# Optimization experiments

Measured on AMD Instinct MI355X. Metric: run time of the kernel, lower is better.

## Reference

```python
import jax, jax.numpy as jnp
import numpy as np

N_NODES = 100000


def gcn_conv(x, edge_index, W, b):
    """PyG GCNConv: linear transform, add self-loops, sym-normalized scatter-add, bias."""
    n = x.shape[0]
    h = x @ W  # [N, out]
    loop = jnp.arange(n, dtype=edge_index.dtype)
    src = jnp.concatenate([edge_index[0], loop])
    dst = jnp.concatenate([edge_index[1], loop])
    deg = jax.ops.segment_sum(jnp.ones_like(dst, dtype=h.dtype), dst, num_segments=n)
    dinv = jnp.where(deg > 0, jax.lax.rsqrt(jnp.maximum(deg, 1.0)), 0.0)
    norm = dinv[src] * dinv[dst]  # [E+N]
    msg = norm[:, None] * h[src]  # gather + scale
    out = jax.ops.segment_sum(msg, dst, num_segments=n)  # scatter-add
    return out + b


def setup_inputs() -> dict:
    key = jax.random.key(0)
    k1, k2, k3, k4 = jax.random.split(key, 4)
    in_f, gnn_f, out_f = 128, 64, 40
    n_edges = 1600000
    x = jax.random.normal(k1, (N_NODES, in_f), dtype=jnp.float32)
    edge_index = jax.random.randint(k2, (2, n_edges), 0, N_NODES, dtype=jnp.int64)
    W1 = jax.random.normal(k3, (in_f, gnn_f), dtype=jnp.float32) * (in_f ** -0.5)
    b1 = jnp.zeros((gnn_f,), dtype=jnp.float32)
    W2 = jax.random.normal(k4, (gnn_f, out_f), dtype=jnp.float32) * (gnn_f ** -0.5)
    b2 = jnp.zeros((out_f,), dtype=jnp.float32)
    return {"x": x, "edge_index": edge_index, "W1": W1, "b1": b1, "W2": W2, "b2": b2}


def reference(x, edge_index, W1, b1, W2, b2):
    h = gcn_conv(x, edge_index, W1, b1)
    h = jax.nn.relu(h)  # Dropout is identity in eval mode
    out = gcn_conv(h, edge_index, W2, b2)
    return out
```

## Files before the change

### kernel.cpp

```cpp
#include <hip/hip_runtime.h>


__device__ inline float bflo(unsigned u) { return __uint_as_float(u << 16); }
__device__ inline float bfhi(unsigned u) { return __uint_as_float(u & 0xffff0000u); }
__device__ inline unsigned short f2bf(float x) {
    unsigned u = __float_as_uint(x);
    return (unsigned short)((u + 0x7fff + ((u >> 16) & 1)) >> 16);
}

#define NBINS 256
#define EPB   2048

__global__ __launch_bounds__(256) void p1_hist(const int* __restrict__ dst, int e,
                                               int nblk, int* __restrict__ hist_t) {
    __shared__ int h[NBINS];
    int tid = threadIdx.x;
    h[tid] = 0;
    __syncthreads();
    int base = blockIdx.x * EPB;
    #pragma unroll
    for (int j = 0; j < 8; ++j) {
        int idx = base + j * 256 + tid;
        if (idx < e) atomicAdd(&h[dst[idx] >> 9], 1);
    }
    __syncthreads();
    hist_t[tid * nblk + blockIdx.x] = h[tid];
}

__global__ __launch_bounds__(256) void scan_a(const int* __restrict__ in, int* __restrict__ part,
                                              int* __restrict__ aux, int n) {
    __shared__ int lds[256];
    int tid = threadIdx.x;
    int base = blockIdx.x * 1024 + tid * 4;
    int v0 = (base + 0 < n) ? in[base + 0] : 0;
    int v1 = (base + 1 < n) ? in[base + 1] : 0;
    int v2 = (base + 2 < n) ? in[base + 2] : 0;
    int v3 = (base + 3 < n) ? in[base + 3] : 0;
    int s = v0 + v1 + v2 + v3;
    lds[tid] = s;
    __syncthreads();
    for (int off = 1; off < 256; off <<= 1) {
        int t = (tid >= off) ? lds[tid - off] : 0;
        __syncthreads();
        lds[tid] += t;
        __syncthreads();
    }
    int excl = lds[tid] - s;
    if (base + 0 < n) part[base + 0] = excl;
    if (base + 1 < n) part[base + 1] = excl + v0;
    if (base + 2 < n) part[base + 2] = excl + v0 + v1;
    if (base + 3 < n) part[base + 3] = excl + v0 + v1 + v2;
    if (tid == 255) aux[blockIdx.x] = lds[255];
}

__global__ __launch_bounds__(256) void scan_b(int* __restrict__ aux, int nb) {
    __shared__ int lds[256];
    int tid = threadIdx.x;
    int v = (tid < nb) ? aux[tid] : 0;
    lds[tid] = v;
    __syncthreads();
    for (int off = 1; off < 256; off <<= 1) {
        int t = (tid >= off) ? lds[tid - off] : 0;
        __syncthreads();
        lds[tid] += t;
        __syncthreads();
    }
    if (tid < nb) aux[tid] = lds[tid] - v;
}

__global__ __launch_bounds__(256) void scan_c(int* __restrict__ data,
                                              const int* __restrict__ aux, int n) {
    int i = blockIdx.x * blockDim.x + threadIdx.x;
    if (i < n) data[i] += aux[i >> 10];
}

__global__ __launch_bounds__(256) void p1_scatter(const int* __restrict__ src,
                                                  const int* __restrict__ dst, int e,
                                                  int nblk, const int* __restrict__ off_t,
                                                  unsigned* __restrict__ ebuf) {
    __shared__ int cur[NBINS];
    int tid = threadIdx.x;
    cur[tid] = off_t[tid * nblk + blockIdx.x];
    __syncthreads();
    int base = blockIdx.x * EPB;
    #pragma unroll
    for (int j = 0; j < 8; ++j) {
        int idx = base + j * 256 + tid;
        if (idx < e) {
            int d = dst[idx];
            int p = atomicAdd(&cur[d >> 9], 1);
            ebuf[p] = (unsigned)src[idx] | ((unsigned)(d & 511) << 17);
        }
    }
}

__global__ __launch_bounds__(256) void p2_build(const unsigned* __restrict__ ebuf,
                                                const int* __restrict__ off_t,
                                                int nblk, int e, int n, int nbg,
                                                int* __restrict__ row_off,
                                                int* __restrict__ ssrc,
                                                float* __restrict__ dinv) {
    __shared__ int cnt[512];
    __shared__ int s1[256];
    __shared__ int loc[512];
    int tid = threadIdx.x;
    int g = blockIdx.x;
    int node0 = g << 9;
    int nlocal = n - node0; if (nlocal > 512) nlocal = 512;

    int segstart = off_t[g * nblk];
    int segend   = (g + 1 < NBINS) ? off_t[(g + 1) * nblk] : e;

    cnt[tid] = 0; cnt[tid + 256] = 0;
    __syncthreads();

    for (int i = segstart + tid; i < segend; i += 256)
        atomicAdd(&cnt[ebuf[i] >> 17], 1);
    __syncthreads();

    int a0 = cnt[2 * tid], a1 = cnt[2 * tid + 1];
    int sp = a0 + a1;
    s1[tid] = sp;
    __syncthreads();
    for (int off = 1; off < 256; off <<= 1) {
        int t = (tid >= off) ? s1[tid - off] : 0;
        __syncthreads();
        s1[tid] += t;
        __syncthreads();
    }
    int excl = s1[tid] - sp;
    loc[2 * tid]     = excl;
    loc[2 * tid + 1] = excl + a0;
    __syncthreads();

    for (int l = tid; l < nlocal; l += 256) {
        row_off[node0 + l] = segstart + loc[l];
        dinv[node0 + l] = rsqrtf((float)cnt[l] + 1.0f);
    }
    if (g == nbg - 1 && tid == 0) row_off[n] = segend;
    __syncthreads();

    for (int i = segstart + tid; i < segend; i += 256) {
        unsigned p = ebuf[i];
        int r = atomicAdd(&loc[p >> 17], 1);
        ssrc[segstart + r] = (int)(p & 0x1FFFFu);
    }
}

template <int K, int M>
__global__ __launch_bounds__(256) void gemm_xw(const float* __restrict__ X,
                                               const float* __restrict__ W,
                                               const float* __restrict__ dinv,
                                               unsigned short* __restrict__ G, int n) {
    constexpr int GQ = 8;
    constexpr int SG = GQ + 1;
    __shared__ float4 xs[64 * SG];
    __shared__ float4 wt[64 * SG];

    const int tid = threadIdx.x;
    const int r0  = blockIdx.x * 64;
    const int tc  = tid & 15;
    const int tr  = tid >> 4;

    const int srow0 = tid >> 3, skq0 = tid & 7;
    const int srow1 = (tid + 256) >> 3, skq1 = tid & 7;
    int rr0 = r0 + srow0; rr0 = rr0 < n ? rr0 : n - 1;
    int rr1 = r0 + srow1; rr1 = rr1 < n ? rr1 : n - 1;

    float acc[4][4];
    #pragma unroll
    for (int i = 0; i < 4; ++i)
        #pragma unroll
        for (int j = 0; j < 4; ++j) acc[i][j] = 0.f;

    for (int kc = 0; kc < K; kc += 32) {
        __syncthreads();
        xs[srow0 * SG + skq0] = *reinterpret_cast<const float4*>(&X[(size_t)rr0 * K + kc + skq0 * 4]);
        xs[srow1 * SG + skq1] = *reinterpret_cast<const float4*>(&X[(size_t)rr1 * K + kc + skq1 * 4]);
        {
            int m = srow0, kq = skq0;
            float4 v = make_float4(0.f, 0.f, 0.f, 0.f);
            if (m < M) {
                int k = kc + kq * 4;
                v.x = W[(k + 0) * M + m]; v.y = W[(k + 1) * M + m];
                v.z = W[(k + 2) * M + m]; v.w = W[(k + 3) * M + m];
            }
            wt[m * SG + kq] = v;
            m = srow1; kq = skq1;
            float4 u = make_float4(0.f, 0.f, 0.f, 0.f);
            if (m < M) {
                int k = kc + kq * 4;
                u.x = W[(k + 0) * M + m]; u.y = W[(k + 1) * M + m];
                u.z = W[(k + 2) * M + m]; u.w = W[(k + 3) * M + m];
            }
            wt[m * SG + kq] = u;
        }
        __syncthreads();

        #pragma unroll 2
        for (int kq = 0; kq < GQ; ++kq) {
            float4 xv[4], wv[4];
            #pragma unroll
            for (int i = 0; i < 4; ++i) xv[i] = xs[(tr + 16 * i) * SG + kq];
            #pragma unroll
            for (int j = 0; j < 4; ++j) wv[j] = wt[(tc + 16 * j) * SG + kq];
            #pragma unroll
            for (int i = 0; i < 4; ++i)
                #pragma unroll
                for (int j = 0; j < 4; ++j) {
                    acc[i][j] = fmaf(xv[i].x, wv[j].x, acc[i][j]);
                    acc[i][j] = fmaf(xv[i].y, wv[j].y, acc[i][j]);
                    acc[i][j] = fmaf(xv[i].z, wv[j].z, acc[i][j]);
                    acc[i][j] = fmaf(xv[i].w, wv[j].w, acc[i][j]);
                }
        }
    }

    #pragma unroll
    for (int i = 0; i < 4; ++i) {
        int row = r0 + tr + 16 * i;
        if (row < n) {
            float di = dinv[row];
            #pragma unroll
            for (int j = 0; j < 4; ++j) {
                int col = tc + 16 * j;
                if (col < M) G[(size_t)row * M + col] = f2bf(di * acc[i][j]);
            }
        }
    }
}

template <bool RELU>
__global__ __launch_bounds__(256) void aggregate64(const unsigned short* __restrict__ G,
                                                   const float* __restrict__ dinv,
                                                   const int* __restrict__ row_off,
                                                   const int* __restrict__ ssrc,
                                                   const float* __restrict__ bias,
                                                   float* __restrict__ out, int n) {
    int wid  = (blockIdx.x * blockDim.x + threadIdx.x) >> 6;
    if (wid >= n) return;
    int lane = threadIdx.x & 63;
    int g = lane >> 3;
    int c = lane & 7;
    const uint4* __restrict__ G16 = (const uint4*)G;

    float acc[8];
    #pragma unroll
    for (int k = 0; k < 8; ++k) acc[k] = 0.f;

    int e0 = row_off[wid], e1 = row_off[wid + 1];
    int e = e0 + g;
    for (; e + 8 < e1; e += 16) {
        int s0 = ssrc[e], s1 = ssrc[e + 8];
        uint4 u0 = G16[(size_t)s0 * 8 + c];
        uint4 u1 = G16[(size_t)s1 * 8 + c];
        acc[0] += bflo(u0.x); acc[1] += bfhi(u0.x);
        acc[2] += bflo(u0.y); acc[3] += bfhi(u0.y);
        acc[4] += bflo(u0.z); acc[5] += bfhi(u0.z);
        acc[6] += bflo(u0.w); acc[7] += bfhi(u0.w);
        acc[0] += bflo(u1.x); acc[1] += bfhi(u1.x);
        acc[2] += bflo(u1.y); acc[3] += bfhi(u1.y);
        acc[4] += bflo(u1.z); acc[5] += bfhi(u1.z);
        acc[6] += bflo(u1.w); acc[7] += bfhi(u1.w);
    }
    if (e < e1) {
        int s = ssrc[e];
        uint4 u = G16[(size_t)s * 8 + c];
        acc[0] += bflo(u.x); acc[1] += bfhi(u.x);
        acc[2] += bflo(u.y); acc[3] += bfhi(u.y);
        acc[4] += bflo(u.z); acc[5] += bfhi(u.z);
        acc[6] += bflo(u.w); acc[7] += bfhi(u.w);
    }

    #pragma unroll
    for (int k = 0; k < 8; ++k) acc[k] += __shfl_xor(acc[k], 8);
    #pragma unroll
    for (int k = 0; k < 8; ++k) acc[k] += __shfl_xor(acc[k], 16);
    #pragma unroll
    for (int k = 0; k < 8; ++k) acc[k] += __shfl_xor(acc[k], 32);

    float di = dinv[wid];
    uint4 gs = G16[(size_t)wid * 8 + c];
    float4 b0 = ((const float4*)bias)[2 * c];
    float4 b1 = ((const float4*)bias)[2 * c + 1];
    float4 o0, o1;
    o0.x = fmaf(di, acc[0] + bflo(gs.x), b0.x);
    o0.y = fmaf(di, acc[1] + bfhi(gs.x), b0.y);
    o0.z = fmaf(di, acc[2] + bflo(gs.y), b0.z);
    o0.w = fmaf(di, acc[3] + bfhi(gs.y), b0.w);
    o1.x = fmaf(di, acc[4] + bflo(gs.z), b1.x);
    o1.y = fmaf(di, acc[5] + bfhi(gs.z), b1.y);
    o1.z = fmaf(di, acc[6] + bflo(gs.w), b1.z);
    o1.w = fmaf(di, acc[7] + bfhi(gs.w), b1.w);
    if (RELU) {
        o0.x = fmaxf(o0.x, 0.f); o0.y = fmaxf(o0.y, 0.f);
        o0.z = fmaxf(o0.z, 0.f); o0.w = fmaxf(o0.w, 0.f);
        o1.x = fmaxf(o1.x, 0.f); o1.y = fmaxf(o1.y, 0.f);
        o1.z = fmaxf(o1.z, 0.f); o1.w = fmaxf(o1.w, 0.f);
    }
    if (g == 0) {
        ((float4*)out)[(size_t)wid * 16 + 2 * c]     = o0;
        ((float4*)out)[(size_t)wid * 16 + 2 * c + 1] = o1;
    }
}

template <bool RELU>
__global__ __launch_bounds__(256) void aggregate40(const unsigned short* __restrict__ G,
                                                   const float* __restrict__ dinv,
                                                   const int* __restrict__ row_off,
                                                   const int* __restrict__ ssrc,
                                                   const float* __restrict__ bias,
                                                   float* __restrict__ out, int n) {
    constexpr int MH = 20;
    int wid  = (blockIdx.x * blockDim.x + threadIdx.x) >> 6;
    if (wid >= n) return;
    int lane = threadIdx.x & 63;
    int half = lane >> 5;
    int c    = lane & 31;
    int cc   = c < MH ? c : MH - 1;
    const unsigned* __restrict__ G2 = (const unsigned*)G;

    float2 acc = make_float2(0.f, 0.f);
    int e0 = row_off[wid], e1 = row_off[wid + 1];

    int e = e0 + half;
    for (; e + 6 < e1; e += 8) {
        int s0 = ssrc[e], s1 = ssrc[e + 2], s2 = ssrc[e + 4], s3 = ssrc[e + 6];
        unsigned g0 = G2[(size_t)s0 * MH + cc];
        unsigned g1 = G2[(size_t)s1 * MH + cc];
        unsigned g2 = G2[(size_t)s2 * MH + cc];
        unsigned g3 = G2[(size_t)s3 * MH + cc];
        acc.x += bflo(g0); acc.y += bfhi(g0);
        acc.x += bflo(g1); acc.y += bfhi(g1);
        acc.x += bflo(g2); acc.y += bfhi(g2);
        acc.x += bflo(g3); acc.y += bfhi(g3);
    }
    for (; e < e1; e += 2) {
        unsigned g = G2[(size_t)ssrc[e] * MH + cc];
        acc.x += bflo(g); acc.y += bfhi(g);
    }

    acc.x += __shfl_xor(acc.x, 32);
    acc.y += __shfl_xor(acc.y, 32);

    float di = dinv[wid];
    unsigned gs = G2[(size_t)wid * MH + cc];
    float2 bv = ((const float2*)bias)[cc];
    float o0 = fmaf(di, acc.x + bflo(gs), bv.x);
    float o1 = fmaf(di, acc.y + bfhi(gs), bv.y);
    if (RELU) { o0 = fmaxf(o0, 0.f); o1 = fmaxf(o1, 0.f); }
    if (half == 0 && c < MH) {
        ((float2*)out)[(size_t)wid * MH + c] = make_float2(o0, o1);
    }
}

extern "C" void kernel_launch(void* const* d_in, const int* in_sizes, int n_in,
                              void* d_out, int out_size, void* d_ws, size_t ws_size,
                              hipStream_t stream) {
    const float* x  = (const float*)d_in[0];
    const int*   ei = (const int*)d_in[1];
    const float* W1 = (const float*)d_in[2];
    const float* b1 = (const float*)d_in[3];
    const float* W2 = (const float*)d_in[4];
    const float* b2 = (const float*)d_in[5];

    const int gnn_f = in_sizes[3];
    const int out_f = in_sizes[5];
    const int in_f  = in_sizes[2] / gnn_f;
    const int e     = in_sizes[1] / 2;
    const int n     = in_sizes[0] / in_f;

    const int* src = ei;
    const int* dst = ei + e;

    const int nblk   = (e + EPB - 1) / EPB;
    const int nscan  = NBINS * nblk;
    const int nbg    = (n + 511) / 512;
    const int nchunks = (nscan + 1023) / 1024;

    char* base = (char*)d_ws;
    size_t off = 0;
    auto alloc = [&](size_t bytes) -> char* {
        char* p = base + off;
        off = (off + bytes + 255) & ~(size_t)255;
        return p;
    };
    int*            hist_t  = (int*)            alloc((size_t)nscan * 4);
    int*            off_t   = (int*)            alloc((size_t)nscan * 4);
    int*            aux     = (int*)            alloc(256 * 4);
    unsigned*       ebuf    = (unsigned*)       alloc((size_t)e * 4);
    int*            row_off = (int*)            alloc((size_t)(n + 1) * 4);
    int*            ssrc    = (int*)            alloc((size_t)e * 4);
    float*          dinv    = (float*)          alloc((size_t)n * 4);
    unsigned short* g1      = (unsigned short*) alloc((size_t)n * gnn_f * 2);
    float*          a1      = (float*)          alloc((size_t)n * gnn_f * 4);
    unsigned short* g2      = (unsigned short*) alloc((size_t)n * out_f * 2);
    (void)ws_size;

    p1_hist<<<nblk, 256, 0, stream>>>(dst, e, nblk, hist_t);
    scan_a<<<nchunks, 256, 0, stream>>>(hist_t, off_t, aux, nscan);
    scan_b<<<1, 256, 0, stream>>>(aux, nchunks);
    scan_c<<<(nscan + 255) / 256, 256, 0, stream>>>(off_t, aux, nscan);
    p1_scatter<<<nblk, 256, 0, stream>>>(src, dst, e, nblk, off_t, ebuf);
    p2_build<<<nbg, 256, 0, stream>>>(ebuf, off_t, nblk, e, n, nbg, row_off, ssrc, dinv);

    gemm_xw<128, 64><<<(n + 63) / 64, 256, 0, stream>>>(x, W1, dinv, g1, n);
    aggregate64<true><<<(n + 3) / 4, 256, 0, stream>>>(g1, dinv, row_off, ssrc, b1, a1, n);

    gemm_xw<64, 40><<<(n + 63) / 64, 256, 0, stream>>>(a1, W2, dinv, g2, n);
    aggregate40<false><<<(n + 3) / 4, 256, 0, stream>>>(g2, dinv, row_off, ssrc, b2, (float*)d_out, n);
}
```

Before: 289.8 us.

## Split feature columns into slices so aggregation gathers hit cache-resident tables

The GEMM now writes its bf16 output in column-sliced layout: 4 slices of 16 features for layer 1 and 2 slices of 20 for layer 2. Each aggregation launches one grid per slice, so every pass gathers from a smaller table that is more likely to stay in L2 or the last-level cache. The cost is that edge indices and row offsets are re-read once per slice, each gather is narrower (4-byte instead of 16-byte loads), and more blocks are launched.

Result: slower. 399.7 us (+38.0%).

```diff
diff --git a/kernel.cpp b/kernel.cpp
--- a/kernel.cpp
+++ b/kernel.cpp
@@ -147,7 +147,7 @@
     }
 }
 
-template <int K, int M>
+template <int K, int M, int SF>
 __global__ __launch_bounds__(256) void gemm_xw(const float* __restrict__ X,
                                                const float* __restrict__ W,
                                                const float* __restrict__ dinv,
@@ -223,135 +223,111 @@
             float di = dinv[row];
             #pragma unroll
             for (int j = 0; j < 4; ++j) {
-                int col = tc + 16 * j;
-                if (col < M) G[(size_t)row * M + col] = f2bf(di * acc[i][j]);
+                int cc = tc + 16 * j;
+                if (cc < M) {
+                    int s  = cc / SF;
+                    int lc = cc - s * SF;
+                    G[(size_t)s * n * SF + (size_t)row * SF + lc] = f2bf(di * acc[i][j]);
+                }
             }
         }
     }
 }
 
 template <bool RELU>
-__global__ __launch_bounds__(256) void aggregate64(const unsigned short* __restrict__ G,
-                                                   const float* __restrict__ dinv,
-                                                   const int* __restrict__ row_off,
-                                                   const int* __restrict__ ssrc,
-                                                   const float* __restrict__ bias,
-                                                   float* __restrict__ out, int n) {
-    int wid  = (blockIdx.x * blockDim.x + threadIdx.x) >> 6;
+__global__ __launch_bounds__(256) void aggregate64s(const unsigned* __restrict__ G,
+                                                    const float* __restrict__ dinv,
+                                                    const int* __restrict__ row_off,
+                                                    const int* __restrict__ ssrc,
+                                                    const float* __restrict__ bias,
+                                                    float* __restrict__ out, int n) {
+    int bps   = (n + 3) >> 2;
+    int slice = blockIdx.x / bps;
+    int blk   = blockIdx.x - slice * bps;
+    int wid   = (blk * 256 + (int)threadIdx.x) >> 6;
     if (wid >= n) return;
     int lane = threadIdx.x & 63;
     int g = lane >> 3;
     int c = lane & 7;
-    const uint4* __restrict__ G16 = (const uint4*)G;
-
-    float acc[8];
-    #pragma unroll
-    for (int k = 0; k < 8; ++k) acc[k] = 0.f;
-
+    const unsigned* __restrict__ Gs = G + (size_t)slice * n * 8;
+
+    float2 acc = make_float2(0.f, 0.f);
     int e0 = row_off[wid], e1 = row_off[wid + 1];
     int e = e0 + g;
     for (; e + 8 < e1; e += 16) {
         int s0 = ssrc[e], s1 = ssrc[e + 8];
-        uint4 u0 = G16[(size_t)s0 * 8 + c];
-        uint4 u1 = G16[(size_t)s1 * 8 + c];
-        acc[0] += bflo(u0.x); acc[1] += bfhi(u0.x);
-        acc[2] += bflo(u0.y); acc[3] += bfhi(u0.y);
-        acc[4] += bflo(u0.z); acc[5] += bfhi(u0.z);
-        acc[6] += bflo(u0.w); acc[7] += bfhi(u0.w);
-        acc[0] += bflo(u1.x); acc[1] += bfhi(u1.x);
-        acc[2] += bflo(u1.y); acc[3] += bfhi(u1.y);
-        acc[4] += bflo(u1.z); acc[5] += bfhi(u1.z);
-        acc[6] += bflo(u1.w); acc[7] += bfhi(u1.w);
+        unsigned u0 = Gs[(size_t)s0 * 8 + c];
+        unsigned u1 = Gs[(size_t)s1 * 8 + c];
+        acc.x += bflo(u0); acc.y += bfhi(u0);
+        acc.x += bflo(u1); acc.y += bfhi(u1);
     }
     if (e < e1) {
-        int s = ssrc[e];
-        uint4 u = G16[(size_t)s * 8 + c];
-        acc[0] += bflo(u.x); acc[1] += bfhi(u.x);
-        acc[2] += bflo(u.y); acc[3] += bfhi(u.y);
-        acc[4] += bflo(u.z); acc[5] += bfhi(u.z);
-        acc[6] += bflo(u.w); acc[7] += bfhi(u.w);
-    }
-
-    #pragma unroll
-    for (int k = 0; k < 8; ++k) acc[k] += __shfl_xor(acc[k], 8);
-    #pragma unroll
-    for (int k = 0; k < 8; ++k) acc[k] += __shfl_xor(acc[k], 16);
-    #pragma unroll
-    for (int k = 0; k < 8; ++k) acc[k] += __shfl_xor(acc[k], 32);
+        unsigned u = Gs[(size_t)ssrc[e] * 8 + c];
+        acc.x += bflo(u); acc.y += bfhi(u);
+    }
+
+    acc.x += __shfl_xor(acc.x, 8);  acc.y += __shfl_xor(acc.y, 8);
+    acc.x += __shfl_xor(acc.x, 16); acc.y += __shfl_xor(acc.y, 16);
+    acc.x += __shfl_xor(acc.x, 32); acc.y += __shfl_xor(acc.y, 32);
 
     float di = dinv[wid];
-    uint4 gs = G16[(size_t)wid * 8 + c];
-    float4 b0 = ((const float4*)bias)[2 * c];
-    float4 b1 = ((const float4*)bias)[2 * c + 1];
-    float4 o0, o1;
-    o0.x = fmaf(di, acc[0] + bflo(gs.x), b0.x);
-    o0.y = fmaf(di, acc[1] + bfhi(gs.x), b0.y);
-    o0.z = fmaf(di, acc[2] + bflo(gs.y), b0.z);
-    o0.w = fmaf(di, acc[3] + bfhi(gs.y), b0.w);
-    o1.x = fmaf(di, acc[4] + bflo(gs.z), b1.x);
-    o1.y = fmaf(di, acc[5] + bfhi(gs.z), b1.y);
-    o1.z = fmaf(di, acc[6] + bflo(gs.w), b1.z);
-    o1.w = fmaf(di, acc[7] + bfhi(gs.w), b1.w);
-    if (RELU) {
-        o0.x = fmaxf(o0.x, 0.f); o0.y = fmaxf(o0.y, 0.f);
-        o0.z = fmaxf(o0.z, 0.f); o0.w = fmaxf(o0.w, 0.f);
-        o1.x = fmaxf(o1.x, 0.f); o1.y = fmaxf(o1.y, 0.f);
-        o1.z = fmaxf(o1.z, 0.f); o1.w = fmaxf(o1.w, 0.f);
-    }
-    if (g == 0) {
-        ((float4*)out)[(size_t)wid * 16 + 2 * c]     = o0;
-        ((float4*)out)[(size_t)wid * 16 + 2 * c + 1] = o1;
-    }
+    unsigned us = Gs[(size_t)wid * 8 + c];
+    float2 bv = ((const float2*)bias)[slice * 8 + c];
+    float2 o;
+    o.x = fmaf(di, acc.x + bflo(us), bv.x);
+    o.y = fmaf(di, acc.y + bfhi(us), bv.y);
+    if (RELU) { o.x = fmaxf(o.x, 0.f); o.y = fmaxf(o.y, 0.f); }
+    if (g == 0) ((float2*)out)[(size_t)wid * 32 + slice * 8 + c] = o;
 }
 
 template <bool RELU>
-__global__ __launch_bounds__(256) void aggregate40(const unsigned short* __restrict__ G,
-                                                   const float* __restrict__ dinv,
-                                                   const int* __restrict__ row_off,
-                                                   const int* __restrict__ ssrc,
-                                                   const float* __restrict__ bias,
-                                                   float* __restrict__ out, int n) {
-    constexpr int MH = 20;
-    int wid  = (blockIdx.x * blockDim.x + threadIdx.x) >> 6;
+__global__ __launch_bounds__(256) void aggregate40s(const unsigned* __restrict__ G,
+                                                    const float* __restrict__ dinv,
+                                                    const int* __restrict__ row_off,
+                                                    const int* __restrict__ ssrc,
+                                                    const float* __restrict__ bias,
+                                                    float* __restrict__ out, int n) {
+    int bps   = (n + 3) >> 2;
+    int slice = blockIdx.x / bps;
+    int blk   = blockIdx.x - slice * bps;
+    int wid   = (blk * 256 + (int)threadIdx.x) >> 6;
     if (wid >= n) return;
     int lane = threadIdx.x & 63;
-    int half = lane >> 5;
-    int c    = lane & 31;
-    int cc   = c < MH ? c : MH - 1;
-    const unsigned* __restrict__ G2 = (const unsigned*)G;
+    int g = lane >> 4;
+    int c = lane & 15;
+    int cc = c < 10 ? c : 9;
+    const unsigned* __restrict__ Gs = G + (size_t)slice * n * 10;
 
     float2 acc = make_float2(0.f, 0.f);
     int e0 = row_off[wid], e1 = row_off[wid + 1];
-
-    int e = e0 + half;
-    for (; e + 6 < e1; e += 8) {
-        int s0 = ssrc[e], s1 = ssrc[e + 2], s2 = ssrc[e + 4], s3 = ssrc[e + 6];
-        unsigned g0 = G2[(size_t)s0 * MH + cc];
-        unsigned g1 = G2[(size_t)s1 * MH + cc];
-        unsigned g2 = G2[(size_t)s2 * MH + cc];
-        unsigned g3 = G2[(size_t)s3 * MH + cc];
-        acc.x += bflo(g0); acc.y += bfhi(g0);
-        acc.x += bflo(g1); acc.y += bfhi(g1);
-        acc.x += bflo(g2); acc.y += bfhi(g2);
-        acc.x += bflo(g3); acc.y += bfhi(g3);
-    }
-    for (; e < e1; e += 2) {
-        unsigned g = G2[(size_t)ssrc[e] * MH + cc];
-        acc.x += bflo(g); acc.y += bfhi(g);
-    }
-
-    acc.x += __shfl_xor(acc.x, 32);
-    acc.y += __shfl_xor(acc.y, 32);
+    int e = e0 + g;
+    for (; e + 12 < e1; e += 16) {
+        int s0 = ssrc[e], s1 = ssrc[e + 4], s2 = ssrc[e + 8], s3 = ssrc[e + 12];
+        unsigned u0 = Gs[(size_t)s0 * 10 + cc];
+        unsigned u1 = Gs[(size_t)s1 * 10 + cc];
+        unsigned u2 = Gs[(size_t)s2 * 10 + cc];
+        unsigned u3 = Gs[(size_t)s3 * 10 + cc];
+        acc.x += bflo(u0); acc.y += bfhi(u0);
+        acc.x += bflo(u1); acc.y += bfhi(u1);
+        acc.x += bflo(u2); acc.y += bfhi(u2);
+        acc.x += bflo(u3); acc.y += bfhi(u3);
+    }
+    for (; e < e1; e += 4) {
+        unsigned u = Gs[(size_t)ssrc[e] * 10 + cc];
+        acc.x += bflo(u); acc.y += bfhi(u);
+    }
+
+    acc.x += __shfl_xor(acc.x, 16); acc.y += __shfl_xor(acc.y, 16);
+    acc.x += __shfl_xor(acc.x, 32); acc.y += __shfl_xor(acc.y, 32);
 
     float di = dinv[wid];
-    unsigned gs = G2[(size_t)wid * MH + cc];
-    float2 bv = ((const float2*)bias)[cc];
-    float o0 = fmaf(di, acc.x + bflo(gs), bv.x);
-    float o1 = fmaf(di, acc.y + bfhi(gs), bv.y);
-    if (RELU) { o0 = fmaxf(o0, 0.f); o1 = fmaxf(o1, 0.f); }
-    if (half == 0 && c < MH) {
-        ((float2*)out)[(size_t)wid * MH + c] = make_float2(o0, o1);
-    }
+    unsigned us = Gs[(size_t)wid * 10 + cc];
+    float2 bv = ((const float2*)bias)[slice * 10 + cc];
+    float2 o;
+    o.x = fmaf(di, acc.x + bflo(us), bv.x);
+    o.y = fmaf(di, acc.y + bfhi(us), bv.y);
+    if (RELU) { o.x = fmaxf(o.x, 0.f); o.y = fmaxf(o.y, 0.f); }
+    if (g == 0 && c < 10) ((float2*)out)[(size_t)wid * 20 + slice * 10 + c] = o;
 }
 
 extern "C" void kernel_launch(void* const* d_in, const int* in_sizes, int n_in,
@@ -377,6 +353,7 @@
     const int nscan  = NBINS * nblk;
     const int nbg    = (n + 511) / 512;
     const int nchunks = (nscan + 1023) / 1024;
+    const int bps    = (n + 3) / 4;
 
     char* base = (char*)d_ws;
     size_t off = 0;
@@ -404,9 +381,9 @@
     p1_scatter<<<nblk, 256, 0, stream>>>(src, dst, e, nblk, off_t, ebuf);
     p2_build<<<nbg, 256, 0, stream>>>(ebuf, off_t, nblk, e, n, nbg, row_off, ssrc, dinv);
 
-    gemm_xw<128, 64><<<(n + 63) / 64, 256, 0, stream>>>(x, W1, dinv, g1, n);
-    aggregate64<true><<<(n + 3) / 4, 256, 0, stream>>>(g1, dinv, row_off, ssrc, b1, a1, n);
-
-    gemm_xw<64, 40><<<(n + 63) / 64, 256, 0, stream>>>(a1, W2, dinv, g2, n);
-    aggregate40<false><<<(n + 3) / 4, 256, 0, stream>>>(g2, dinv, row_off, ssrc, b2, (float*)d_out, n);
-}
+    gemm_xw<128, 64, 16><<<(n + 63) / 64, 256, 0, stream>>>(x, W1, dinv, g1, n);
+    aggregate64s<true><<<4 * bps, 256, 0, stream>>>((const unsigned*)g1, dinv, row_off, ssrc, b1, a1, n);
+
+    gemm_xw<64, 40, 20><<<(n + 63) / 64, 256, 0, stream>>>(a1, W2, dinv, g2, n);
+    aggregate40s<false><<<2 * bps, 256, 0, stream>>>((const unsigned*)g2, dinv, row_off, ssrc, b2, (float*)d_out, n);
+}
```
